# Kernel optimization log

Measured on AMD Instinct MI355X. Metric: run time of the kernel, lower is better.

## Reference

```python
import jax, jax.numpy as jnp
import numpy as np

M, K, N, G = 8192, 4096, 11008, 128  # tokens, in_features, out_features, quant groups (group_size=32)


def setup_inputs() -> dict:
    key = jax.random.key(0)
    k1, k2, k3, k4 = jax.random.split(key, 4)
    A = jax.random.normal(k1, (M, K), dtype=jnp.float32)
    # packed int4 weights: two nibbles per uint8 byte along K
    weight = jax.random.randint(k2, (K // 2, N), 0, 256, dtype=jnp.int32).astype(jnp.uint8)
    # per-group, per-output-channel dequant scales (positive, small)
    weight_scale = jax.random.uniform(k3, (G, N), dtype=jnp.float32, minval=0.005, maxval=0.02)
    bias = jax.random.normal(k4, (N,), dtype=jnp.float32) * 0.01
    return {"A": A, "weight": weight, "weight_scale": weight_scale, "bias": bias}


def unpack_int4(x, x_scale):
    # x: uint8 [K//2, N]; x_scale: float [G, N] -> float [K, N]
    Kd = x.shape[0] * 2
    Gd, Nd = x_scale.shape
    group_k = Kd // Gd
    # row 2i = low nibble, row 2i+1 = high nibble (matches shifts [0, 4])
    nib = jnp.stack([x & 15, (x >> 4) & 15], axis=1).reshape(Kd, Nd)
    w = (nib.astype(jnp.int8) - 8).astype(x_scale.dtype)
    return (w.reshape(Gd, group_k, Nd) * x_scale[:, None, :]).reshape(Kd, Nd)


def reference(A, weight, weight_scale, bias):
    # out = A @ dequant(weight) + bias
    W = unpack_int4(weight, weight_scale)
    return A @ W + bias
```

## Files before the change

kernel.cpp:

```cpp
#include <hip/hip_runtime.h>
#include <hip/hip_bf16.h>
#include <stdint.h>

typedef __attribute__((ext_vector_type(8))) short bf16x8;
typedef __attribute__((ext_vector_type(4))) float f32x4;
typedef __attribute__((ext_vector_type(4))) int i32x4;

constexpr int Mdim = 8192;
constexpr int Ndim = 11008;
constexpr int Kdim = 4096;
constexpr int NT = Kdim / 64;
constexpr int NWG = (Mdim / 256) * (Ndim / 256);
constexpr int CPX = NWG / 8;
constexpr int NBN = Ndim / 256;

__device__ __forceinline__ unsigned short f2bf(float f) {
    __bf16 h = (__bf16)f;
    return __builtin_bit_cast(unsigned short, h);
}

__device__ __forceinline__ void gload16(const void* g, void* lds) {
    __builtin_amdgcn_global_load_lds(
        (const __attribute__((address_space(1))) unsigned int*)g,
        (__attribute__((address_space(3))) unsigned int*)lds,
        16, 0, 0);
}

__global__ __launch_bounds__(256) void prepAS_kernel(const float* __restrict__ A,
                                                     char* __restrict__ Aq,
                                                     float* __restrict__ sA,
                                                     const float* __restrict__ Ws,
                                                     float* __restrict__ Fc,
                                                     float* __restrict__ sCol)
{
    const int tid = threadIdx.x;
    if (blockIdx.x >= Mdim) {
        const int n = (blockIdx.x - Mdim) * 256 + tid;
        float mx = 0.f;
        for (int g = 0; g < 128; ++g) mx = fmaxf(mx, Ws[(size_t)g * Ndim + n]);
        Fc[n]   = 15.875f / mx;
        sCol[n] = mx * (8.0f / 127.0f);
        return;
    }
    __shared__ float red[4];
    const int row = blockIdx.x;
    const float* src = A + (size_t)row * Kdim + tid * 16;
    f32x4 v[4];
    float m = 0.f;
#pragma unroll
    for (int j = 0; j < 4; ++j) {
        v[j] = *(const f32x4*)(src + j * 4);
#pragma unroll
        for (int e = 0; e < 4; ++e) m = fmaxf(m, fabsf(v[j][e]));
    }
#pragma unroll
    for (int o = 32; o > 0; o >>= 1) m = fmaxf(m, __shfl_down(m, o));
    if ((tid & 63) == 0) red[tid >> 6] = m;
    __syncthreads();
    m = fmaxf(fmaxf(red[0], red[1]), fmaxf(red[2], red[3]));
    const float inv = 127.0f / m;
    if (tid == 0) sA[row] = m * (1.0f / 127.0f);
    char out[16];
#pragma unroll
    for (int j = 0; j < 4; ++j)
#pragma unroll
        for (int e = 0; e < 4; ++e)
            out[j * 4 + e] = (char)__float2int_rn(v[j][e] * inv);
    *(i32x4*)(Aq + (size_t)row * Kdim + tid * 16) = *(const i32x4*)out;
}

__global__ __launch_bounds__(256) void wq_kernel(const int* __restrict__ Wq,
                                                 const float* __restrict__ Ws,
                                                 const float* __restrict__ Fc,
                                                 char* __restrict__ Wt)
{
    __shared__ char T[64][80];
    const int kt = blockIdx.x % (Kdim / 64);
    const int nt = blockIdx.x / (Kdim / 64);
    const int k0 = kt * 64, n0 = nt * 64;
    const int t = threadIdx.x;

    const int pr   = t >> 3;
    const int nloc = (t & 7) * 8;
    const int* wp = Wq + (size_t)(k0 / 2 + pr) * Ndim + n0 + nloc;
    const i32x4 ra = *(const i32x4*)wp;
    const i32x4 rb = *(const i32x4*)(wp + 4);
    const int g = (k0 + 2 * pr) >> 5;
    const float* sp = Ws + (size_t)g * Ndim + n0 + nloc;
    const f32x4 s0 = *(const f32x4*)sp;
    const f32x4 s1 = *(const f32x4*)(sp + 4);
    const f32x4 f0 = *(const f32x4*)(Fc + n0 + nloc);
    const f32x4 f1 = *(const f32x4*)(Fc + n0 + nloc + 4);
#pragma unroll
    for (int i = 0; i < 8; ++i) {
        const int v = (i < 4) ? ra[i] : rb[i - 4];
        const float sf = ((i < 4) ? s0[i] : s1[i - 4]) * ((i < 4) ? f0[i] : f1[i - 4]);
        T[nloc + i][2 * pr]     = (char)__float2int_rn((float)((v & 15) - 8) * sf);
        T[nloc + i][2 * pr + 1] = (char)__float2int_rn((float)(((v >> 4) & 15) - 8) * sf);
    }
    __syncthreads();
    const int nl = t >> 2;
    const int ko = (t & 3) * 16;
    const i32x4 o = *(const i32x4*)&T[nl][ko];
    *(i32x4*)(Wt + (size_t)(n0 + nl) * Kdim + k0 + ko) = o;
}

__global__ __launch_bounds__(512, 2) void gemm_i8_kernel(
    const char* __restrict__ Ab,
    const char* __restrict__ Bt,
    const float* __restrict__ sA,
    const float* __restrict__ sCol,
    const float* __restrict__ Bias,
    float* __restrict__ Out)
{
    __shared__ char sh[65536];

    const int tid  = threadIdx.x;
    const int lane = tid & 63;
    const int wid  = tid >> 6;
    const int wr   = wid >> 2;
    const int wc   = wid & 3;
    const int l15  = lane & 15;
    const int l4   = lane >> 4;
    const int rcol = ((l4 ^ ((l15 >> 1) & 3)) << 4);

    const int wg  = ((int)blockIdx.x % 8) * CPX + (int)blockIdx.x / 8;
    const int bm = wg / NBN, bn = wg % NBN;
    const int m0 = bm * 256, n0 = bn * 256;

    const int sr   = tid >> 2;
    const int sc16 = ((tid & 3) ^ ((tid >> 3) & 3)) * 16;
    const int ldo  = tid * 16;
    const char* aSrc = Ab + (size_t)(m0 + sr) * Kdim + sc16;
    const char* bSrc = Bt + (size_t)(n0 + sr) * Kdim + sc16;

    auto stageA = [&](int tt, int h, int slot) {
        gload16(aSrc + (size_t)(h * 128) * Kdim + tt * 64, &sh[slot * 8192 + ldo]);
    };
    auto stageB = [&](int tt, int h, int slot) {
        gload16(bSrc + (size_t)(h * 128) * Kdim + tt * 64, &sh[32768 + slot * 8192 + ldo]);
    };

    i32x4 acc[8][4];
#pragma unroll
    for (int i = 0; i < 8; ++i)
#pragma unroll
        for (int j = 0; j < 4; ++j) acc[i][j] = (i32x4){0, 0, 0, 0};

    stageA(0, 0, 0); stageA(0, 1, 1);
    stageB(0, 0, 0); stageB(0, 1, 1);
    stageB(1, 0, 2); stageB(1, 1, 3);
    asm volatile("s_waitcnt vmcnt(2)" ::: "memory");
    __builtin_amdgcn_s_barrier();

    const int browb = (wc & 1) * 64;

    for (int t = 0; t < NT; ++t) {
        const int par = t & 1, parn = par ^ 1;
        const char* aslot = &sh[(par * 2 + wr) * 8192];
        const char* bslot = &sh[32768 + (par * 2 + (wc >> 1)) * 8192];

        i32x4 bv[4], av[8];
#pragma unroll
        for (int fn = 0; fn < 4; ++fn)
            bv[fn] = *(const i32x4*)&bslot[(browb + fn * 16 + l15) * 64 + rcol];
#pragma unroll
        for (int fm = 0; fm < 8; ++fm)
            av[fm] = *(const i32x4*)&aslot[(fm * 16 + l15) * 64 + rcol];

        if (t + 1 < NT) { stageA(t + 1, 0, parn * 2 + 0); stageA(t + 1, 1, parn * 2 + 1); }

        __builtin_amdgcn_s_setprio(1);
#pragma unroll
        for (int fm = 0; fm < 4; ++fm)
#pragma unroll
            for (int fn = 0; fn < 4; ++fn)
                acc[fm][fn] = __builtin_amdgcn_mfma_i32_16x16x64_i8(
                    av[fm], bv[fn], acc[fm][fn], 0, 0, 0);
        __builtin_amdgcn_s_setprio(0);

        asm volatile("" ::: "memory");
        __builtin_amdgcn_s_barrier();

        if (t + 2 < NT) { stageB(t + 2, 0, par * 2 + 0); stageB(t + 2, 1, par * 2 + 1); }

        __builtin_amdgcn_s_setprio(1);
#pragma unroll
        for (int fm = 4; fm < 8; ++fm)
#pragma unroll
            for (int fn = 0; fn < 4; ++fn)
                acc[fm][fn] = __builtin_amdgcn_mfma_i32_16x16x64_i8(
                    av[fm], bv[fn], acc[fm][fn], 0, 0, 0);
        __builtin_amdgcn_s_setprio(0);

        if (t < NT - 2)       asm volatile("s_waitcnt vmcnt(2)" ::: "memory");
        else if (t == NT - 2) asm volatile("s_waitcnt vmcnt(0)" ::: "memory");
        asm volatile("" ::: "memory");
        __builtin_amdgcn_s_barrier();
    }

    const int rb = l4 * 4;
    float sc[4], bb[4];
#pragma unroll
    for (int fn = 0; fn < 4; ++fn) {
        const int ng = n0 + wc * 64 + fn * 16 + l15;
        sc[fn] = sCol[ng];
        bb[fn] = Bias[ng];
    }
#pragma unroll
    for (int fm = 0; fm < 8; ++fm) {
        const size_t mg = (size_t)(m0 + wr * 128 + fm * 16 + rb);
#pragma unroll
        for (int r = 0; r < 4; ++r) {
            const float sa = sA[mg + r];
#pragma unroll
            for (int fn = 0; fn < 4; ++fn) {
                const int ng = n0 + wc * 64 + fn * 16 + l15;
                __builtin_nontemporal_store((float)acc[fm][fn][r] * sa * sc[fn] + bb[fn],
                                            &Out[(mg + r) * Ndim + ng]);
            }
        }
    }
}

constexpr int SA = 72;
__global__ __launch_bounds__(256) void w4a32_fused_kernel(
    const float* __restrict__ A,
    const int* __restrict__ Wq,
    const float* __restrict__ Ws,
    const float* __restrict__ Bias,
    float* __restrict__ Out)
{
    __shared__ unsigned short As[128 * SA];
    __shared__ unsigned short Bs[128 * SA];
    const int tid = threadIdx.x;
    const int nbn = Ndim / 128;
    const int bn = blockIdx.x % nbn;
    const int bm = blockIdx.x / nbn;
    const int m0 = bm * 128, n0 = bn * 128;
    const int lane = tid & 63;
    const int wid  = tid >> 6;
    const int wr   = wid >> 1;
    const int wc   = wid & 1;
    const int l15  = lane & 15;
    const int l4   = lane >> 4;
    f32x4 acc[4][4];
#pragma unroll
    for (int i = 0; i < 4; ++i)
#pragma unroll
        for (int j = 0; j < 4; ++j) acc[i][j] = (f32x4){0.f, 0.f, 0.f, 0.f};
    const int a_tr = tid >> 3;
    const int a_tc = (tid & 7) * 8;
    const int kp2  = tid >> 4;
    const int n8   = (tid & 15) * 8;
    for (int kt = 0; kt < Kdim / 64; ++kt) {
        const int k0 = kt * 64;
        __syncthreads();
#pragma unroll
        for (int j = 0; j < 4; ++j) {
            const int ml = a_tr + 32 * j;
            const float* src = A + (size_t)(m0 + ml) * Kdim + (k0 + a_tc);
            const f32x4 x0 = *(const f32x4*)src;
            const f32x4 x1 = *(const f32x4*)(src + 4);
            union { bf16x8 v; unsigned short u[8]; } h;
            h.u[0] = f2bf(x0[0]); h.u[1] = f2bf(x0[1]);
            h.u[2] = f2bf(x0[2]); h.u[3] = f2bf(x0[3]);
            h.u[4] = f2bf(x1[0]); h.u[5] = f2bf(x1[1]);
            h.u[6] = f2bf(x1[2]); h.u[7] = f2bf(x1[3]);
            *(bf16x8*)(&As[ml * SA + (a_tc ^ ((ml & 7) << 3))]) = h.v;
        }
        {
            const int pr = kt * 32 + 2 * kp2;
            const int* wp = Wq + (size_t)pr * Ndim + (n0 + n8);
            const i32x4 r0a = *(const i32x4*)wp;
            const i32x4 r0b = *(const i32x4*)(wp + 4);
            const i32x4 r1a = *(const i32x4*)(wp + Ndim);
            const i32x4 r1b = *(const i32x4*)(wp + Ndim + 4);
            const int g = 2 * kt + (kp2 >> 3);
            const float* sp = Ws + (size_t)g * Ndim + (n0 + n8);
            const f32x4 s0 = *(const f32x4*)sp;
            const f32x4 s1 = *(const f32x4*)(sp + 4);
#pragma unroll
            for (int i = 0; i < 8; ++i) {
                const float s = (i < 4) ? s0[i] : s1[i - 4];
                const int b0 = (i < 4) ? r0a[i] : r0b[i - 4];
                const int b1 = (i < 4) ? r1a[i] : r1b[i - 4];
                union { unsigned long long v; unsigned short u[4]; } o;
                o.u[0] = f2bf((float)((b0 & 15) - 8) * s);
                o.u[1] = f2bf((float)(((b0 >> 4) & 15) - 8) * s);
                o.u[2] = f2bf((float)((b1 & 15) - 8) * s);
                o.u[3] = f2bf((float)(((b1 >> 4) & 15) - 8) * s);
                const int nl = n8 + i;
                const int swzz = ((nl ^ (nl >> 3)) & 7) << 3;
                *(unsigned long long*)(&Bs[nl * SA + ((4 * kp2) ^ swzz)]) = o.v;
            }
        }
        __syncthreads();
#pragma unroll
        for (int ks = 0; ks < 2; ++ks) {
            const int kb  = ks * 32 + l4 * 8;
            const int swa = (l15 & 7) << 3;
            bf16x8 af[4], bfr[4];
#pragma unroll
            for (int fm = 0; fm < 4; ++fm) {
                const int row = wr * 64 + fm * 16 + l15;
                af[fm] = *(const bf16x8*)(&As[row * SA + (kb ^ swa)]);
            }
#pragma unroll
            for (int fn = 0; fn < 4; ++fn) {
                const int nrow = wc * 64 + fn * 16 + l15;
                const int swb = ((nrow ^ (nrow >> 3)) & 7) << 3;
                bfr[fn] = *(const bf16x8*)(&Bs[nrow * SA + (kb ^ swb)]);
            }
#pragma unroll
            for (int fm = 0; fm < 4; ++fm)
#pragma unroll
                for (int fn = 0; fn < 4; ++fn)
                    acc[fm][fn] = __builtin_amdgcn_mfma_f32_16x16x32_bf16(
                        af[fm], bfr[fn], acc[fm][fn], 0, 0, 0);
        }
    }
    const int rb = l4 * 4;
    float bv[4];
#pragma unroll
    for (int fn = 0; fn < 4; ++fn)
        bv[fn] = Bias[n0 + wc * 64 + fn * 16 + l15];
#pragma unroll
    for (int fm = 0; fm < 4; ++fm) {
        const size_t mg = (size_t)(m0 + wr * 64 + fm * 16 + rb);
#pragma unroll
        for (int fn = 0; fn < 4; ++fn) {
            const int ng = n0 + wc * 64 + fn * 16 + l15;
            const float b = bv[fn];
#pragma unroll
            for (int r = 0; r < 4; ++r)
                Out[(mg + r) * Ndim + ng] = acc[fm][fn][r] + b;
        }
    }
}

extern "C" void kernel_launch(void* const* d_in, const int* in_sizes, int n_in,
                              void* d_out, int out_size, void* d_ws, size_t ws_size,
                              hipStream_t stream) {
    const float* A    = (const float*)d_in[0];
    const int* Wq     = (const int*)d_in[1];
    const float* Ws   = (const float*)d_in[2];
    const float* Bias = (const float*)d_in[3];
    float* Out        = (float*)d_out;

    const size_t offAq = 0;
    const size_t offWt = (size_t)Mdim * Kdim;
    const size_t offSA = offWt + (size_t)Ndim * Kdim;
    const size_t offF  = offSA + (size_t)Mdim * 4;
    const size_t offSC = offF + (size_t)Ndim * 4;
    const size_t need  = offSC + (size_t)Ndim * 4;

    if (ws_size >= need) {
        char*  Aq   = (char*)d_ws + offAq;
        char*  Wt   = (char*)d_ws + offWt;
        float* sAp  = (float*)((char*)d_ws + offSA);
        float* Fc   = (float*)((char*)d_ws + offF);
        float* sCol = (float*)((char*)d_ws + offSC);
        prepAS_kernel<<<Mdim + Ndim / 256, 256, 0, stream>>>(A, Aq, sAp, Ws, Fc, sCol);
        wq_kernel<<<(Kdim / 64) * (Ndim / 64), 256, 0, stream>>>(Wq, Ws, Fc, Wt);
        gemm_i8_kernel<<<NWG, 512, 0, stream>>>(Aq, Wt, sAp, sCol, Bias, Out);
    } else {
        w4a32_fused_kernel<<<(Mdim / 128) * (Ndim / 128), 256, 0, stream>>>(A, Wq, Ws, Bias, Out);
    }
}
```

Measured before the change: 490.9 us.

## Restructure int8 GEMM to 4 waves with 128x128 warp tiles and 4-stage pipeline

```diff
diff --git a/kernel.cpp b/kernel.cpp
--- a/kernel.cpp
+++ b/kernel.cpp
@@ -105,7 +105,7 @@
     *(i32x4*)(Wt + (size_t)(n0 + nl) * Kdim + k0 + ko) = o;
 }
 
-__global__ __launch_bounds__(512, 2) void gemm_i8_kernel(
+__global__ __launch_bounds__(256, 1) void gemm_i8_kernel(
     const char* __restrict__ Ab,
     const char* __restrict__ Bt,
     const float* __restrict__ sA,
@@ -113,13 +113,13 @@
     const float* __restrict__ Bias,
     float* __restrict__ Out)
 {
-    __shared__ char sh[65536];
+    __shared__ char sh[131072];
 
     const int tid  = threadIdx.x;
     const int lane = tid & 63;
     const int wid  = tid >> 6;
-    const int wr   = wid >> 2;
-    const int wc   = wid & 3;
+    const int wr   = wid >> 1;
+    const int wc   = wid & 1;
     const int l15  = lane & 15;
     const int l4   = lane >> 4;
     const int rcol = ((l4 ^ ((l15 >> 1) & 3)) << 4);
@@ -134,76 +134,73 @@
     const char* aSrc = Ab + (size_t)(m0 + sr) * Kdim + sc16;
     const char* bSrc = Bt + (size_t)(n0 + sr) * Kdim + sc16;
 
-    auto stageA = [&](int tt, int h, int slot) {
-        gload16(aSrc + (size_t)(h * 128) * Kdim + tt * 64, &sh[slot * 8192 + ldo]);
+    auto stageA = [&](int tt) {
+        char* base = &sh[(tt & 3) * 16384 + ldo];
+#pragma unroll
+        for (int j = 0; j < 4; ++j)
+            gload16(aSrc + (size_t)(j * 64) * Kdim + tt * 64, base + j * 4096);
     };
-    auto stageB = [&](int tt, int h, int slot) {
-        gload16(bSrc + (size_t)(h * 128) * Kdim + tt * 64, &sh[32768 + slot * 8192 + ldo]);
+    auto stageB = [&](int tt) {
+        char* base = &sh[65536 + (tt & 3) * 16384 + ldo];
+#pragma unroll
+        for (int j = 0; j < 4; ++j)
+            gload16(bSrc + (size_t)(j * 64) * Kdim + tt * 64, base + j * 4096);
     };
 
-    i32x4 acc[8][4];
+#define READF(TT, AF, BF)                                                     \
+    {                                                                         \
+        const char* as_ = &sh[((TT) & 3) * 16384];                            \
+        const char* bs_ = &sh[65536 + ((TT) & 3) * 16384];                    \
+        _Pragma("unroll")                                                     \
+        for (int f = 0; f < 8; ++f)                                           \
+            AF[f] = *(const i32x4*)&as_[(wr * 128 + f * 16 + l15) * 64 + rcol]; \
+        _Pragma("unroll")                                                     \
+        for (int f = 0; f < 8; ++f)                                           \
+            BF[f] = *(const i32x4*)&bs_[(wc * 128 + f * 16 + l15) * 64 + rcol]; \
+    }
+
+    i32x4 acc[8][8];
 #pragma unroll
     for (int i = 0; i < 8; ++i)
 #pragma unroll
-        for (int j = 0; j < 4; ++j) acc[i][j] = (i32x4){0, 0, 0, 0};
-
-    stageA(0, 0, 0); stageA(0, 1, 1);
-    stageB(0, 0, 0); stageB(0, 1, 1);
-    stageB(1, 0, 2); stageB(1, 1, 3);
-    asm volatile("s_waitcnt vmcnt(2)" ::: "memory");
+        for (int j = 0; j < 8; ++j) acc[i][j] = (i32x4){0, 0, 0, 0};
+
+    stageA(0); stageB(0);
+    stageA(1); stageB(1);
+    stageA(2); stageB(2);
+    asm volatile("s_waitcnt vmcnt(8)" ::: "memory");
     __builtin_amdgcn_s_barrier();
 
-    const int browb = (wc & 1) * 64;
-
-    for (int t = 0; t < NT; ++t) {
-        const int par = t & 1, parn = par ^ 1;
-        const char* aslot = &sh[(par * 2 + wr) * 8192];
-        const char* bslot = &sh[32768 + (par * 2 + (wc >> 1)) * 8192];
-
-        i32x4 bv[4], av[8];
-#pragma unroll
-        for (int fn = 0; fn < 4; ++fn)
-            bv[fn] = *(const i32x4*)&bslot[(browb + fn * 16 + l15) * 64 + rcol];
-#pragma unroll
-        for (int fm = 0; fm < 8; ++fm)
-            av[fm] = *(const i32x4*)&aslot[(fm * 16 + l15) * 64 + rcol];
-
-        if (t + 1 < NT) { stageA(t + 1, 0, parn * 2 + 0); stageA(t + 1, 1, parn * 2 + 1); }
-
-        __builtin_amdgcn_s_setprio(1);
-#pragma unroll
-        for (int fm = 0; fm < 4; ++fm)
-#pragma unroll
-            for (int fn = 0; fn < 4; ++fn)
-                acc[fm][fn] = __builtin_amdgcn_mfma_i32_16x16x64_i8(
-                    av[fm], bv[fn], acc[fm][fn], 0, 0, 0);
-        __builtin_amdgcn_s_setprio(0);
-
-        asm volatile("" ::: "memory");
-        __builtin_amdgcn_s_barrier();
-
-        if (t + 2 < NT) { stageB(t + 2, 0, par * 2 + 0); stageB(t + 2, 1, par * 2 + 1); }
-
-        __builtin_amdgcn_s_setprio(1);
-#pragma unroll
-        for (int fm = 4; fm < 8; ++fm)
-#pragma unroll
-            for (int fn = 0; fn < 4; ++fn)
-                acc[fm][fn] = __builtin_amdgcn_mfma_i32_16x16x64_i8(
-                    av[fm], bv[fn], acc[fm][fn], 0, 0, 0);
-        __builtin_amdgcn_s_setprio(0);
-
-        if (t < NT - 2)       asm volatile("s_waitcnt vmcnt(2)" ::: "memory");
-        else if (t == NT - 2) asm volatile("s_waitcnt vmcnt(0)" ::: "memory");
-        asm volatile("" ::: "memory");
-        __builtin_amdgcn_s_barrier();
+    i32x4 aF0[8], bF0[8], aF1[8], bF1[8];
+    READF(0, aF0, bF0);
+
+#define BODY(T, CA, CB, NA, NB)                                               \
+    {                                                                         \
+        if ((T) + 1 < NT) READF((T) + 1, NA, NB);                             \
+        if ((T) + 3 < NT) { stageA((T) + 3); stageB((T) + 3); }               \
+        _Pragma("unroll")                                                     \
+        for (int fm = 0; fm < 8; ++fm) {                                      \
+            _Pragma("unroll")                                                 \
+            for (int fn = 0; fn < 8; ++fn)                                    \
+                acc[fm][fn] = __builtin_amdgcn_mfma_i32_16x16x64_i8(          \
+                    CA[fm], CB[fn], acc[fm][fn], 0, 0, 0);                    \
+        }                                                                     \
+        if ((T) <= NT - 4)      asm volatile("s_waitcnt vmcnt(8)" ::: "memory"); \
+        else if ((T) == NT - 3) asm volatile("s_waitcnt vmcnt(0)" ::: "memory"); \
+        asm volatile("" ::: "memory");                                        \
+        __builtin_amdgcn_s_barrier();                                         \
+    }
+
+    for (int t2 = 0; t2 < NT; t2 += 2) {
+        BODY(t2,     aF0, bF0, aF1, bF1);
+        BODY(t2 + 1, aF1, bF1, aF0, bF0);
     }
 
     const int rb = l4 * 4;
-    float sc[4], bb[4];
-#pragma unroll
-    for (int fn = 0; fn < 4; ++fn) {
-        const int ng = n0 + wc * 64 + fn * 16 + l15;
+    float sc[8], bb[8];
+#pragma unroll
+    for (int fn = 0; fn < 8; ++fn) {
+        const int ng = n0 + wc * 128 + fn * 16 + l15;
         sc[fn] = sCol[ng];
         bb[fn] = Bias[ng];
     }
@@ -214,13 +211,15 @@
         for (int r = 0; r < 4; ++r) {
             const float sa = sA[mg + r];
 #pragma unroll
-            for (int fn = 0; fn < 4; ++fn) {
-                const int ng = n0 + wc * 64 + fn * 16 + l15;
+            for (int fn = 0; fn < 8; ++fn) {
+                const int ng = n0 + wc * 128 + fn * 16 + l15;
                 __builtin_nontemporal_store((float)acc[fm][fn][r] * sa * sc[fn] + bb[fn],
                                             &Out[(mg + r) * Ndim + ng]);
             }
         }
     }
+#undef READF
+#undef BODY
 }
 
 constexpr int SA = 72;
@@ -363,7 +362,7 @@
         float* sCol = (float*)((char*)d_ws + offSC);
         prepAS_kernel<<<Mdim + Ndim / 256, 256, 0, stream>>>(A, Aq, sAp, Ws, Fc, sCol);
         wq_kernel<<<(Kdim / 64) * (Ndim / 64), 256, 0, stream>>>(Wq, Ws, Fc, Wt);
-        gemm_i8_kernel<<<NWG, 512, 0, stream>>>(Aq, Wt, sAp, sCol, Bias, Out);
+        gemm_i8_kernel<<<NWG, 256, 0, stream>>>(Aq, Wt, sAp, sCol, Bias, Out);
     } else {
         w4a32_fused_kernel<<<(Mdim / 128) * (Ndim / 128), 256, 0, stream>>>(A, Wq, Ws, Bias, Out);
     }
```

After: 1.072 ms. 118% more time.

## Shrink int8 GEMM workgroup tile to 256x128 with four waves

Applied to the files above, without the earlier changes.

```diff
diff --git a/kernel.cpp b/kernel.cpp
--- a/kernel.cpp
+++ b/kernel.cpp
@@ -10,9 +10,9 @@
 constexpr int Ndim = 11008;
 constexpr int Kdim = 4096;
 constexpr int NT = Kdim / 64;
-constexpr int NWG = (Mdim / 256) * (Ndim / 256);
+constexpr int NWG = (Mdim / 256) * (Ndim / 128);
 constexpr int CPX = NWG / 8;
-constexpr int NBN = Ndim / 256;
+constexpr int NBN = Ndim / 128;
 
 __device__ __forceinline__ unsigned short f2bf(float f) {
     __bf16 h = (__bf16)f;
@@ -105,7 +105,7 @@
     *(i32x4*)(Wt + (size_t)(n0 + nl) * Kdim + k0 + ko) = o;
 }
 
-__global__ __launch_bounds__(512, 2) void gemm_i8_kernel(
+__global__ __launch_bounds__(256, 3) void gemm_i8_kernel(
     const char* __restrict__ Ab,
     const char* __restrict__ Bt,
     const float* __restrict__ sA,
@@ -113,20 +113,20 @@
     const float* __restrict__ Bias,
     float* __restrict__ Out)
 {
-    __shared__ char sh[65536];
+    __shared__ char sh[49152];
 
     const int tid  = threadIdx.x;
     const int lane = tid & 63;
     const int wid  = tid >> 6;
-    const int wr   = wid >> 2;
-    const int wc   = wid & 3;
+    const int wr   = wid >> 1;
+    const int wc   = wid & 1;
     const int l15  = lane & 15;
     const int l4   = lane >> 4;
     const int rcol = ((l4 ^ ((l15 >> 1) & 3)) << 4);
 
     const int wg  = ((int)blockIdx.x % 8) * CPX + (int)blockIdx.x / 8;
     const int bm = wg / NBN, bn = wg % NBN;
-    const int m0 = bm * 256, n0 = bn * 256;
+    const int m0 = bm * 256, n0 = bn * 128;
 
     const int sr   = tid >> 2;
     const int sc16 = ((tid & 3) ^ ((tid >> 3) & 3)) * 16;
@@ -134,11 +134,17 @@
     const char* aSrc = Ab + (size_t)(m0 + sr) * Kdim + sc16;
     const char* bSrc = Bt + (size_t)(n0 + sr) * Kdim + sc16;
 
-    auto stageA = [&](int tt, int h, int slot) {
-        gload16(aSrc + (size_t)(h * 128) * Kdim + tt * 64, &sh[slot * 8192 + ldo]);
+    auto stageA = [&](int tt) {
+        char* base = &sh[(tt & 1) * 16384 + ldo];
+#pragma unroll
+        for (int j = 0; j < 4; ++j)
+            gload16(aSrc + (size_t)(j * 64) * Kdim + tt * 64, base + j * 4096);
     };
-    auto stageB = [&](int tt, int h, int slot) {
-        gload16(bSrc + (size_t)(h * 128) * Kdim + tt * 64, &sh[32768 + slot * 8192 + ldo]);
+    auto stageB = [&](int tt) {
+        char* base = &sh[32768 + (tt & 1) * 8192 + ldo];
+#pragma unroll
+        for (int j = 0; j < 2; ++j)
+            gload16(bSrc + (size_t)(j * 64) * Kdim + tt * 64, base + j * 4096);
     };
 
     i32x4 acc[8][4];
@@ -147,28 +153,25 @@
 #pragma unroll
         for (int j = 0; j < 4; ++j) acc[i][j] = (i32x4){0, 0, 0, 0};
 
-    stageA(0, 0, 0); stageA(0, 1, 1);
-    stageB(0, 0, 0); stageB(0, 1, 1);
-    stageB(1, 0, 2); stageB(1, 1, 3);
+    stageA(0); stageB(0);
+    stageB(1);
     asm volatile("s_waitcnt vmcnt(2)" ::: "memory");
     __builtin_amdgcn_s_barrier();
 
-    const int browb = (wc & 1) * 64;
-
     for (int t = 0; t < NT; ++t) {
         const int par = t & 1, parn = par ^ 1;
-        const char* aslot = &sh[(par * 2 + wr) * 8192];
-        const char* bslot = &sh[32768 + (par * 2 + (wc >> 1)) * 8192];
+        const char* aslot = &sh[par * 16384];
+        const char* bslot = &sh[32768 + par * 8192];
 
         i32x4 bv[4], av[8];
 #pragma unroll
         for (int fn = 0; fn < 4; ++fn)
-            bv[fn] = *(const i32x4*)&bslot[(browb + fn * 16 + l15) * 64 + rcol];
+            bv[fn] = *(const i32x4*)&bslot[(wc * 64 + fn * 16 + l15) * 64 + rcol];
 #pragma unroll
         for (int fm = 0; fm < 8; ++fm)
-            av[fm] = *(const i32x4*)&aslot[(fm * 16 + l15) * 64 + rcol];
-
-        if (t + 1 < NT) { stageA(t + 1, 0, parn * 2 + 0); stageA(t + 1, 1, parn * 2 + 1); }
+            av[fm] = *(const i32x4*)&aslot[(wr * 128 + fm * 16 + l15) * 64 + rcol];
+
+        if (t + 1 < NT) stageA(t + 1);
 
         __builtin_amdgcn_s_setprio(1);
 #pragma unroll
@@ -182,7 +185,7 @@
         asm volatile("" ::: "memory");
         __builtin_amdgcn_s_barrier();
 
-        if (t + 2 < NT) { stageB(t + 2, 0, par * 2 + 0); stageB(t + 2, 1, par * 2 + 1); }
+        if (t + 2 < NT) stageB(t + 2);
 
         __builtin_amdgcn_s_setprio(1);
 #pragma unroll
@@ -363,7 +366,7 @@
         float* sCol = (float*)((char*)d_ws + offSC);
         prepAS_kernel<<<Mdim + Ndim / 256, 256, 0, stream>>>(A, Aq, sAp, Ws, Fc, sCol);
         wq_kernel<<<(Kdim / 64) * (Ndim / 64), 256, 0, stream>>>(Wq, Ws, Fc, Wt);
-        gemm_i8_kernel<<<NWG, 512, 0, stream>>>(Aq, Wt, sAp, sCol, Bias, Out);
+        gemm_i8_kernel<<<NWG, 256, 0, stream>>>(Aq, Wt, sAp, sCol, Bias, Out);
     } else {
         w4a32_fused_kernel<<<(Mdim / 128) * (Ndim / 128), 256, 0, stream>>>(A, Wq, Ws, Bias, Out);
     }
```

After: 1.221 ms. 149% more time.
